# Optimization experiments

Measured on AMD Instinct MI355X. Metric: run time of the kernel, lower is better.

The kernel has to match this reference:

```python
import jax, jax.numpy as jnp
import numpy as np

N_HEAD = 16


def _rope(x, cos, sin):
    # x: [B, T, H, hd]; cos/sin: [1, T, 1, hd//2] (interleaved-pair rotation)
    x1, x2 = x[..., ::2], x[..., 1::2]
    r1 = x1 * cos - x2 * sin
    r2 = x1 * sin + x2 * cos
    return jnp.stack([r1, r2], axis=-1).reshape(x.shape)


def setup_inputs() -> dict:
    key = jax.random.key(0)
    k1, k2, k3 = jax.random.split(key, 3)
    B, T, D = 2, 2048, 2048
    x = jax.random.normal(k1, (B, T, D), dtype=jnp.float32)
    w_attn = jax.random.normal(k2, (3 * D, D), dtype=jnp.float32) * 0.02
    w_proj = jax.random.normal(k3, (D, D), dtype=jnp.float32) * 0.02
    return {"x": x, "w_attn": w_attn, "w_proj": w_proj}


def reference(x, w_attn, w_proj):
    B, T, D = x.shape
    H = N_HEAD
    hd = D // H
    # fused QKV projection (bias=False)
    qkv = x @ w_attn.T                      # [B, T, 3D]
    q, k, v = jnp.split(qkv, 3, axis=-1)
    q = q.reshape(B, T, H, hd)
    k = k.reshape(B, T, H, hd)
    v = v.reshape(B, T, H, hd)
    # RoPE tables: inv_freq = 1/10000^(2i/hd), angles m*theta_i
    inv_freq = 1.0 / (10000.0 ** (jnp.arange(0, hd, 2, dtype=jnp.float32) / hd))
    t = jnp.arange(T, dtype=jnp.float32)
    freqs = t[:, None] * inv_freq[None, :]  # [T, hd//2]
    cos = jnp.cos(freqs)[None, :, None, :]
    sin = jnp.sin(freqs)[None, :, None, :]
    q = _rope(q, cos, sin)
    k = _rope(k, cos, sin)
    # causal attention with materialized [B,H,T,T] scores (as in source)
    scale = 1.0 / np.sqrt(hd).astype(np.float32)
    att = jnp.einsum('bthd,bshd->bhts', q, k) * scale
    causal = jnp.tril(jnp.ones((T, T), dtype=bool))
    att = jnp.where(causal, att, -jnp.inf)
    att = jax.nn.softmax(att, axis=-1)
    y = jnp.einsum('bhts,bshd->bthd', att, v).reshape(B, T, D)
    return y @ w_proj.T
```

## Files before the change

### kernel.cpp

```cpp
#include <hip/hip_runtime.h>
#include <hip/hip_bf16.h>

#define T_SEQ 2048
#define DMODEL 2048
#define NB 2
#define NH 16
#define HD 128

typedef __attribute__((ext_vector_type(8))) short short8;
typedef __attribute__((ext_vector_type(4))) float f32x4;
typedef __attribute__((ext_vector_type(16))) float f32x16;
typedef unsigned short ushort_t;

__device__ inline ushort_t f2bf(float f) {
  union { float f; unsigned u; } v; v.f = f;
  unsigned r = v.u + 0x7fffu + ((v.u >> 16) & 1u);
  return (ushort_t)(r >> 16);
}
__device__ inline float bf2f(ushort_t u) {
  union { unsigned u; float f; } v; v.u = ((unsigned)u) << 16;
  return v.f;
}
__device__ inline unsigned pk2(float x, float y) {
  union { __hip_bfloat162 h; unsigned u; } c;
  c.h = __float22bfloat162_rn(float2{x, y});
  return c.u;
}
__device__ inline float fexp2(float x) {
  float r;
  asm("v_exp_f32 %0, %1" : "=v"(r) : "v"(x));
  return r;
}

__device__ inline void gload16(const void* g, void* l) {
  __builtin_amdgcn_global_load_lds(
      (const __attribute__((address_space(1))) unsigned*)g,
      (__attribute__((address_space(3))) unsigned*)l, 16, 0, 0);
}

__global__ void cvt_f32_bf16(const float* __restrict__ src, ushort_t* __restrict__ dst, int n8) {
  int i = blockIdx.x * blockDim.x + threadIdx.x;
  if (i >= n8) return;
  const float4* s = (const float4*)src + (size_t)i * 2;
  float4 a = s[0], b = s[1];
  short8 o;
  o[0] = (short)f2bf(a.x); o[1] = (short)f2bf(a.y);
  o[2] = (short)f2bf(a.z); o[3] = (short)f2bf(a.w);
  o[4] = (short)f2bf(b.x); o[5] = (short)f2bf(b.y);
  o[6] = (short)f2bf(b.z); o[7] = (short)f2bf(b.w);
  *((short8*)dst + i) = o;
}

__global__ void trig_init(float* __restrict__ trig) {
  int idx = blockIdx.x * blockDim.x + threadIdx.x;
  if (idx >= T_SEQ * 64) return;
  int i = idx & 63, t = idx >> 6;
  float inv = __expf(-(float)i * (9.210340371976184f / 64.0f));
  float f = (float)t * inv;
  trig[idx * 2]     = cosf(f);
  trig[idx * 2 + 1] = sinf(f);
}

__global__ void rope_kernel(ushort_t* __restrict__ q, ushort_t* __restrict__ k,
                            const float* __restrict__ trig) {
  int idx = blockIdx.x * blockDim.x + threadIdx.x;
  int i8 = idx & 15;
  int h  = (idx >> 4) & 15;
  int t  = (idx >> 8) & (T_SEQ - 1);
  int b  = idx >> 19;
  size_t base = ((size_t)((b * NH + h) * T_SEQ + t)) * HD + i8 * 8;
  const float4* tr = (const float4*)(trig + t * 128 + i8 * 8);
  float4 t0 = tr[0], t1 = tr[1];
  float c[4] = { t0.x, t0.z, t1.x, t1.z };
  float s[4] = { t0.y, t0.w, t1.y, t1.w };
  short8 vq = *(short8*)(q + base);
  short8 vk = *(short8*)(k + base);
  short8 oq, ok;
#pragma unroll
  for (int j = 0; j < 4; ++j) {
    float x1 = bf2f((ushort_t)vq[2*j]), x2 = bf2f((ushort_t)vq[2*j+1]);
    oq[2*j]   = (short)f2bf(x1 * c[j] - x2 * s[j]);
    oq[2*j+1] = (short)f2bf(x1 * s[j] + x2 * c[j]);
    x1 = bf2f((ushort_t)vk[2*j]); x2 = bf2f((ushort_t)vk[2*j+1]);
    ok[2*j]   = (short)f2bf(x1 * c[j] - x2 * s[j]);
    ok[2*j+1] = (short)f2bf(x1 * s[j] + x2 * c[j]);
  }
  *(short8*)(q + base) = oq;
  *(short8*)(k + base) = ok;
}

__global__ __launch_bounds__(256)
void v_transpose(const ushort_t* __restrict__ v, ushort_t* __restrict__ vt) {
  __shared__ __align__(16) ushort_t L[64][136];
  int bh = blockIdx.y;
  int t0 = blockIdx.x * 64;
  int tid = threadIdx.x;
  int row = tid >> 2, c0 = (tid & 3) * 32;
  const ushort_t* src = v + ((size_t)bh * T_SEQ + t0 + row) * HD + c0;
#pragma unroll
  for (int j = 0; j < 4; ++j)
    *(short8*)&L[row][c0 + j * 8] = *(const short8*)(src + j * 8);
  __syncthreads();
  int d = tid >> 1, tc = (tid & 1) * 32;
  union { ushort_t u[32]; short8 v8[4]; } buf;
#pragma unroll
  for (int j = 0; j < 32; ++j) buf.u[j] = L[tc + j][d];
  ushort_t* dst = vt + ((size_t)bh * HD + d) * T_SEQ + t0 + tc;
#pragma unroll
  for (int j = 0; j < 4; ++j) *(short8*)(dst + j * 8) = buf.v8[j];
}

template <int EPI>
__global__ __launch_bounds__(256)
void gemm_bt(const ushort_t* __restrict__ A, const ushort_t* __restrict__ Bt,
             float* __restrict__ C, ushort_t* __restrict__ q_t,
             ushort_t* __restrict__ k_t, ushort_t* __restrict__ v_t,
             int M, int N, int K) {
  __shared__ __align__(16) ushort_t As[128 * 32];
  __shared__ __align__(16) ushort_t Bs[128 * 32];
  int tid = threadIdx.x, lane = tid & 63, w = tid >> 6;
  int wm = w >> 1, wn = w & 1;
  int li = lane & 15, lg = lane >> 4;
  int tile_n = blockIdx.x * 128, tile_m = blockIdx.y * 128;
  f32x4 acc[4][4] = {};
  int arow = lane >> 2, acol = (lane & 3) * 8;
  const ushort_t* Ag = A + (size_t)tile_m * K;
  const ushort_t* Bg = Bt + (size_t)tile_n * K;
  for (int k0 = 0; k0 < K; k0 += 32) {
#pragma unroll
    for (int i = 0; i < 2; ++i) {
      int blk = w * 2 + i;
      gload16(Ag + (size_t)(blk * 16 + arow) * K + k0 + acol, &As[blk * 512]);
      gload16(Bg + (size_t)(blk * 16 + arow) * K + k0 + acol, &Bs[blk * 512]);
    }
    __syncthreads();
    short8 af[4], bfr[4];
#pragma unroll
    for (int mi = 0; mi < 4; ++mi)
      af[mi] = *(const short8*)&As[(wm * 64 + mi * 16 + li) * 32 + lg * 8];
#pragma unroll
    for (int ni = 0; ni < 4; ++ni)
      bfr[ni] = *(const short8*)&Bs[(wn * 64 + ni * 16 + li) * 32 + lg * 8];
#pragma unroll
    for (int mi = 0; mi < 4; ++mi)
#pragma unroll
      for (int ni = 0; ni < 4; ++ni)
        acc[mi][ni] = __builtin_amdgcn_mfma_f32_16x16x32_bf16(af[mi], bfr[ni], acc[mi][ni], 0, 0, 0);
    __syncthreads();
  }
#pragma unroll
  for (int mi = 0; mi < 4; ++mi) {
    int row = tile_m + wm * 64 + mi * 16 + lg * 4;
#pragma unroll
    for (int ni = 0; ni < 4; ++ni) {
      int col = tile_n + wn * 64 + ni * 16 + li;
#pragma unroll
      for (int r = 0; r < 4; ++r) {
        float val = acc[mi][ni][r];
        if (EPI == 0) {
          C[(size_t)(row + r) * N + col] = val;
        } else {
          int m = row + r;
          int b = m >> 11, t = m & 2047;
          int sec = col >> 11, nn = col & 2047;
          int h = nn >> 7, d = nn & 127;
          ushort_t* dst = (sec == 0) ? q_t : ((sec == 1) ? k_t : v_t);
          dst[((size_t)((b * NH + h) * T_SEQ + t)) * HD + d] = f2bf(val);
        }
      }
    }
  }
}

__global__ __launch_bounds__(256, 2)
void flash_attn(const ushort_t* __restrict__ Q, const ushort_t* __restrict__ Kg,
                const ushort_t* __restrict__ Vt, ushort_t* __restrict__ Y) {
  __shared__ __align__(16) ushort_t ldsK[2 * 64 * 128];
  __shared__ __align__(16) ushort_t ldsV[2 * 128 * 64];
  int tid = threadIdx.x, lane = tid & 63, w = tid >> 6;
  int hi = lane >> 5, l31 = lane & 31;
  int qi = (blockIdx.y & 16) ? (15 - (int)blockIdx.x) : (int)blockIdx.x;
  int bh = blockIdx.y;
  int b = bh >> 4, h = bh & 15;
  int q0 = qi * 128;
  const ushort_t* Qp = Q + (size_t)bh * T_SEQ * HD;
  const ushort_t* Kp = Kg + (size_t)bh * T_SEQ * HD;
  const ushort_t* Vp = Vt + (size_t)bh * HD * T_SEQ;

  int qg = q0 + w * 32 + l31;
  int qmaxw = q0 + w * 32 + 31;

  auto stage = [&](int kv0, int bsel) {
    ushort_t* Kb = ldsK + bsel * 8192;
    ushort_t* Vb = ldsV + bsel * 8192;
#pragma unroll
    for (int p = 0; p < 4; ++p) {
      int c = p * 256 + w * 64 + lane;
      {
        int row = c >> 4, cc = c & 15;
        int sc = cc ^ (row & 15);
        gload16(Kp + (size_t)(kv0 + row) * HD + sc * 8, Kb + (p * 256 + w * 64) * 8);
      }
      {
        int d = c >> 3, cc = c & 7;
        int sc = cc ^ (d & 7);
        gload16(Vp + (size_t)d * T_SEQ + kv0 + sc * 8, Vb + (p * 256 + w * 64) * 8);
      }
    }
  };

  short8 qf[8];
#pragma unroll
  for (int ds = 0; ds < 8; ++ds)
    qf[ds] = *(const short8*)(Qp + (size_t)qg * HD + ds * 16 + hi * 8);

  f32x16 o[4] = {};
  float mu = -1e30f, l = 0.f;
  const float SIG = 0.12751879523209784f;

  int nkt = 2 * qi + 2;
  stage(0, 0);
  __syncthreads();
  int cur = 0;
  for (int kt = 0; kt < nkt; ++kt) {
    int kv0 = kt * 64;
    if (kt + 1 < nkt) stage((kt + 1) * 64, cur ^ 1);
    if (kv0 <= qmaxw) {
      const ushort_t* Kb = ldsK + cur * 8192;
      const ushort_t* Vb = ldsV + cur * 8192;
      f32x16 sa = {}, sb = {};
      __builtin_amdgcn_s_setprio(1);
#pragma unroll
      for (int ds = 0; ds < 8; ++ds) {
        int cc = ds * 2 + hi;
        short8 k0 = *(const short8*)&Kb[l31 * 128 + ((cc ^ (l31 & 15)) * 8)];
        short8 k1 = *(const short8*)&Kb[(32 + l31) * 128 + ((cc ^ (l31 & 15)) * 8)];
        sa = __builtin_amdgcn_mfma_f32_32x32x16_bf16(k0, qf[ds], sa, 0, 0, 0);
        sb = __builtin_amdgcn_mfma_f32_32x32x16_bf16(k1, qf[ds], sb, 0, 0, 0);
      }
      __builtin_amdgcn_s_setprio(0);
      float p[32];
#pragma unroll
      for (int r = 0; r < 16; ++r) { p[r] = sa[r] * SIG; p[16 + r] = sb[r] * SIG; }
      if (kv0 + 63 > qmaxw - 31 + (l31 - l31)) {
        if (kv0 + 63 > q0 + w * 32) {
#pragma unroll
          for (int r = 0; r < 16; ++r) {
            int loc = (r & 3) + 8 * (r >> 2) + 4 * hi;
            if (kv0 + loc > qg)      p[r]      = -3e38f;
            if (kv0 + 32 + loc > qg) p[16 + r] = -3e38f;
          }
        }
      }
      float tm[16];
#pragma unroll
      for (int i = 0; i < 16; ++i) tm[i] = fmaxf(p[i], p[i + 16]);
#pragma unroll
      for (int st = 8; st >= 1; st >>= 1)
#pragma unroll
        for (int i = 0; i < 8; ++i)
          if (i < st) tm[i] = fmaxf(tm[i], tm[i + st]);
      float pmax = fmaxf(tm[0], __shfl_xor(tm[0], 32));
      bool resc = !__all(pmax <= mu + 11.0f);
      if (resc) {
        float munew = fmaxf(mu, pmax);
        float alpha = fexp2(mu - munew);
        mu = munew;
        l *= alpha;
#pragma unroll
        for (int dsub = 0; dsub < 4; ++dsub)
#pragma unroll
          for (int r = 0; r < 16; ++r) o[dsub][r] *= alpha;
      }
#pragma unroll
      for (int i = 0; i < 32; ++i) p[i] = fexp2(p[i] - mu);
      float ts[16];
#pragma unroll
      for (int i = 0; i < 16; ++i) ts[i] = p[i] + p[i + 16];
#pragma unroll
      for (int st = 8; st >= 1; st >>= 1)
#pragma unroll
        for (int i = 0; i < 8; ++i)
          if (i < st) ts[i] += ts[i + st];
      l += ts[0] + __shfl_xor(ts[0], 32);
      __builtin_amdgcn_s_setprio(1);
#pragma unroll
      for (int s = 0; s < 4; ++s) {
        int rb = (s >> 1) * 16 + (s & 1) * 8;
        unsigned a0 = pk2(p[rb + 0], p[rb + 1]);
        unsigned a1 = pk2(p[rb + 2], p[rb + 3]);
        unsigned a2 = pk2(p[rb + 4], p[rb + 5]);
        unsigned a3 = pk2(p[rb + 6], p[rb + 7]);
        unsigned sa0 = (unsigned)__shfl_xor((int)a0, 32);
        unsigned sa1 = (unsigned)__shfl_xor((int)a1, 32);
        unsigned sa2 = (unsigned)__shfl_xor((int)a2, 32);
        unsigned sa3 = (unsigned)__shfl_xor((int)a3, 32);
        union { unsigned u[4]; short8 s8; } pf;
        pf.u[0] = hi ? sa2 : a0;
        pf.u[1] = hi ? sa3 : a1;
        pf.u[2] = hi ? a2 : sa0;
        pf.u[3] = hi ? a3 : sa1;
#pragma unroll
        for (int dsub = 0; dsub < 4; ++dsub) {
          int row = dsub * 32 + l31;
          short8 vf = *(const short8*)&Vb[row * 64 + (((2 * s + hi) ^ (row & 7)) * 8)];
          o[dsub] = __builtin_amdgcn_mfma_f32_32x32x16_bf16(vf, pf.s8, o[dsub], 0, 0, 0);
        }
      }
      __builtin_amdgcn_s_setprio(0);
    }
    __syncthreads();
    cur ^= 1;
  }
  float invl = 1.f / l;
#pragma unroll
  for (int dsub = 0; dsub < 4; ++dsub)
#pragma unroll
    for (int r = 0; r < 16; ++r) o[dsub][r] *= invl;
#pragma unroll
  for (int dsub = 0; dsub < 4; ++dsub)
#pragma unroll
    for (int r = 0; r < 16; r += 2) {
      int d0 = dsub * 32 + (r & 3) + 8 * (r >> 2) + 4 * hi;
      unsigned u = pk2(o[dsub][r], o[dsub][r + 1]);
      *(unsigned*)&ldsK[w * 4096 + l31 * 128 + (((d0 >> 3) ^ (l31 & 15)) * 8) + (d0 & 7)] = u;
    }
  __syncthreads();
#pragma unroll
  for (int rep = 0; rep < 8; ++rep) {
    int idx = rep * 256 + tid;
    int qg2 = idx >> 4, c = idx & 15;
    int wv2 = qg2 >> 5, ql = qg2 & 31;
    short8 val = *(const short8*)&ldsK[wv2 * 4096 + ql * 128 + ((c ^ (ql & 15)) * 8)];
    *(short8*)(Y + ((size_t)(b * T_SEQ + q0 + qg2)) * DMODEL + h * HD + c * 8) = val;
  }
}

extern "C" void kernel_launch(void* const* d_in, const int* in_sizes, int n_in,
                              void* d_out, int out_size, void* d_ws, size_t ws_size,
                              hipStream_t stream) {
  const float* x      = (const float*)d_in[0];
  const float* w_attn = (const float*)d_in[1];
  const float* w_proj = (const float*)d_in[2];
  float* out = (float*)d_out;

  char* ws = (char*)d_ws;
  size_t off = 0;
  auto alloc = [&](size_t bytes) -> void* {
    void* p = ws + off;
    off = (off + bytes + 255) & ~(size_t)255;
    return p;
  };
  const size_t MT = (size_t)NB * T_SEQ;
  ushort_t* xb   = (ushort_t*)alloc(MT * DMODEL * 2);
  ushort_t* wab  = (ushort_t*)alloc((size_t)3 * DMODEL * DMODEL * 2);
  ushort_t* wpb  = (ushort_t*)alloc((size_t)DMODEL * DMODEL * 2);
  ushort_t* q_t  = (ushort_t*)alloc(MT * DMODEL * 2);
  ushort_t* k_t  = (ushort_t*)alloc(MT * DMODEL * 2);
  ushort_t* v_t  = (ushort_t*)alloc(MT * DMODEL * 2);
  ushort_t* vtb  = (ushort_t*)alloc(MT * DMODEL * 2);
  ushort_t* yb   = (ushort_t*)alloc(MT * DMODEL * 2);
  float*    trig = (float*)alloc((size_t)T_SEQ * 64 * 2 * 4);
  (void)ws_size; (void)n_in; (void)in_sizes; (void)out_size;

  {
    int n8x = (int)(MT * DMODEL / 8);
    hipLaunchKernelGGL(cvt_f32_bf16, dim3((n8x + 255) / 256), dim3(256), 0, stream, x, xb, n8x);
    int n8a = (int)((size_t)3 * DMODEL * DMODEL / 8);
    hipLaunchKernelGGL(cvt_f32_bf16, dim3((n8a + 255) / 256), dim3(256), 0, stream, w_attn, wab, n8a);
    int n8p = (int)((size_t)DMODEL * DMODEL / 8);
    hipLaunchKernelGGL(cvt_f32_bf16, dim3((n8p + 255) / 256), dim3(256), 0, stream, w_proj, wpb, n8p);
  }
  hipLaunchKernelGGL(trig_init, dim3(T_SEQ * 64 / 256), dim3(256), 0, stream, trig);

  hipLaunchKernelGGL((gemm_bt<1>), dim3(3 * DMODEL / 128, MT / 128), dim3(256), 0, stream,
                     xb, wab, (float*)nullptr, q_t, k_t, v_t,
                     (int)MT, 3 * DMODEL, DMODEL);

  hipLaunchKernelGGL(rope_kernel, dim3(NB * T_SEQ * NH * 16 / 256), dim3(256), 0, stream,
                     q_t, k_t, trig);

  hipLaunchKernelGGL(v_transpose, dim3(T_SEQ / 64, NB * NH), dim3(256), 0, stream, v_t, vtb);

  hipLaunchKernelGGL(flash_attn, dim3(T_SEQ / 128, NB * NH), dim3(256), 0, stream,
                     q_t, k_t, vtb, yb);

  hipLaunchKernelGGL((gemm_bt<0>), dim3(DMODEL / 128, MT / 128), dim3(256), 0, stream,
                     yb, wpb, out, (ushort_t*)nullptr, (ushort_t*)nullptr, (ushort_t*)nullptr,
                     (int)MT, DMODEL, DMODEL);
}
```

Before: 322.0 us.

## Fuse RoPE and V transpose into the QKV GEMM epilogue

The QKV projection epilogue now applies RoPE to Q and K in registers, using a lane shuffle to fetch the pair partner and reading cos/sin from the trig table. It also writes V already transposed through a swizzled LDS staging buffer. This removes the separate rope and v_transpose kernels and their extra global read/write passes over Q, K and V. The attention mask condition is also simplified. The cost is a heavier GEMM epilogue with scattered trig loads, and RoPE is now applied to fp32 accumulators before rounding to bf16 instead of to already-rounded bf16 values.

After: 317.8 us. About the same (-1.3%).

```diff
diff --git a/kernel.cpp b/kernel.cpp
--- a/kernel.cpp
+++ b/kernel.cpp
@@ -61,63 +61,15 @@
   trig[idx * 2 + 1] = sinf(f);
 }
 
-__global__ void rope_kernel(ushort_t* __restrict__ q, ushort_t* __restrict__ k,
-                            const float* __restrict__ trig) {
-  int idx = blockIdx.x * blockDim.x + threadIdx.x;
-  int i8 = idx & 15;
-  int h  = (idx >> 4) & 15;
-  int t  = (idx >> 8) & (T_SEQ - 1);
-  int b  = idx >> 19;
-  size_t base = ((size_t)((b * NH + h) * T_SEQ + t)) * HD + i8 * 8;
-  const float4* tr = (const float4*)(trig + t * 128 + i8 * 8);
-  float4 t0 = tr[0], t1 = tr[1];
-  float c[4] = { t0.x, t0.z, t1.x, t1.z };
-  float s[4] = { t0.y, t0.w, t1.y, t1.w };
-  short8 vq = *(short8*)(q + base);
-  short8 vk = *(short8*)(k + base);
-  short8 oq, ok;
-#pragma unroll
-  for (int j = 0; j < 4; ++j) {
-    float x1 = bf2f((ushort_t)vq[2*j]), x2 = bf2f((ushort_t)vq[2*j+1]);
-    oq[2*j]   = (short)f2bf(x1 * c[j] - x2 * s[j]);
-    oq[2*j+1] = (short)f2bf(x1 * s[j] + x2 * c[j]);
-    x1 = bf2f((ushort_t)vk[2*j]); x2 = bf2f((ushort_t)vk[2*j+1]);
-    ok[2*j]   = (short)f2bf(x1 * c[j] - x2 * s[j]);
-    ok[2*j+1] = (short)f2bf(x1 * s[j] + x2 * c[j]);
-  }
-  *(short8*)(q + base) = oq;
-  *(short8*)(k + base) = ok;
-}
-
-__global__ __launch_bounds__(256)
-void v_transpose(const ushort_t* __restrict__ v, ushort_t* __restrict__ vt) {
-  __shared__ __align__(16) ushort_t L[64][136];
-  int bh = blockIdx.y;
-  int t0 = blockIdx.x * 64;
-  int tid = threadIdx.x;
-  int row = tid >> 2, c0 = (tid & 3) * 32;
-  const ushort_t* src = v + ((size_t)bh * T_SEQ + t0 + row) * HD + c0;
-#pragma unroll
-  for (int j = 0; j < 4; ++j)
-    *(short8*)&L[row][c0 + j * 8] = *(const short8*)(src + j * 8);
-  __syncthreads();
-  int d = tid >> 1, tc = (tid & 1) * 32;
-  union { ushort_t u[32]; short8 v8[4]; } buf;
-#pragma unroll
-  for (int j = 0; j < 32; ++j) buf.u[j] = L[tc + j][d];
-  ushort_t* dst = vt + ((size_t)bh * HD + d) * T_SEQ + t0 + tc;
-#pragma unroll
-  for (int j = 0; j < 4; ++j) *(short8*)(dst + j * 8) = buf.v8[j];
-}
-
 template <int EPI>
 __global__ __launch_bounds__(256)
 void gemm_bt(const ushort_t* __restrict__ A, const ushort_t* __restrict__ Bt,
              float* __restrict__ C, ushort_t* __restrict__ q_t,
-             ushort_t* __restrict__ k_t, ushort_t* __restrict__ v_t,
-             int M, int N, int K) {
-  __shared__ __align__(16) ushort_t As[128 * 32];
-  __shared__ __align__(16) ushort_t Bs[128 * 32];
+             ushort_t* __restrict__ k_t, ushort_t* __restrict__ vt,
+             const float* __restrict__ trig, int M, int N, int K) {
+  __shared__ __align__(16) ushort_t smem[8192];
+  ushort_t* As = smem;
+  ushort_t* Bs = smem + 4096;
   int tid = threadIdx.x, lane = tid & 63, w = tid >> 6;
   int wm = w >> 1, wn = w & 1;
   int li = lane & 15, lg = lane >> 4;
@@ -148,24 +100,72 @@
         acc[mi][ni] = __builtin_amdgcn_mfma_f32_16x16x32_bf16(af[mi], bfr[ni], acc[mi][ni], 0, 0, 0);
     __syncthreads();
   }
-#pragma unroll
-  for (int mi = 0; mi < 4; ++mi) {
-    int row = tile_m + wm * 64 + mi * 16 + lg * 4;
-#pragma unroll
-    for (int ni = 0; ni < 4; ++ni) {
-      int col = tile_n + wn * 64 + ni * 16 + li;
-#pragma unroll
-      for (int r = 0; r < 4; ++r) {
-        float val = acc[mi][ni][r];
-        if (EPI == 0) {
-          C[(size_t)(row + r) * N + col] = val;
-        } else {
-          int m = row + r;
-          int b = m >> 11, t = m & 2047;
-          int sec = col >> 11, nn = col & 2047;
-          int h = nn >> 7, d = nn & 127;
-          ushort_t* dst = (sec == 0) ? q_t : ((sec == 1) ? k_t : v_t);
-          dst[((size_t)((b * NH + h) * T_SEQ + t)) * HD + d] = f2bf(val);
+
+  if (EPI == 0) {
+#pragma unroll
+    for (int mi = 0; mi < 4; ++mi) {
+      int row = tile_m + wm * 64 + mi * 16 + lg * 4;
+#pragma unroll
+      for (int ni = 0; ni < 4; ++ni) {
+        int col = tile_n + wn * 64 + ni * 16 + li;
+#pragma unroll
+        for (int r = 0; r < 4; ++r)
+          C[(size_t)(row + r) * N + col] = acc[mi][ni][r];
+      }
+    }
+  } else {
+    int sec = tile_n >> 11;
+    int nn  = tile_n & 2047;
+    int h   = nn >> 7;
+    int bq  = tile_m >> 11;
+    int t0  = tile_m & 2047;
+    if (sec < 2) {
+      ushort_t* dst = (sec == 0) ? q_t : k_t;
+      ushort_t* base = dst + ((size_t)(bq * NH + h)) * T_SEQ * HD;
+#pragma unroll
+      for (int mi = 0; mi < 4; ++mi) {
+        int tl = wm * 64 + mi * 16 + lg * 4;
+#pragma unroll
+        for (int ni = 0; ni < 4; ++ni) {
+          int d = wn * 64 + ni * 16 + li;
+          int fi = d >> 1;
+#pragma unroll
+          for (int r = 0; r < 4; ++r) {
+            int t = t0 + tl + r;
+            float val = acc[mi][ni][r];
+            float par = __shfl_xor(val, 1);
+            const float* tp = trig + t * 128 + fi * 2;
+            float c = tp[0], s = tp[1];
+            float out = (li & 1) ? (par * s + val * c) : (val * c - par * s);
+            base[(size_t)t * HD + d] = f2bf(out);
+          }
+        }
+      }
+    } else {
+      ushort_t* vbase = vt + ((size_t)(bq * NH + h)) * HD * T_SEQ;
+#pragma unroll
+      for (int c = 0; c < 2; ++c) {
+        __syncthreads();
+        if (wm == c) {
+#pragma unroll
+          for (int mi = 0; mi < 4; ++mi)
+#pragma unroll
+            for (int ni = 0; ni < 4; ++ni) {
+              int d = wn * 64 + ni * 16 + li;
+#pragma unroll
+              for (int r = 0; r < 4; ++r) {
+                int tl = mi * 16 + lg * 4 + r;
+                smem[d * 64 + (tl ^ ((d & 7) << 3))] = f2bf(acc[mi][ni][r]);
+              }
+            }
+        }
+        __syncthreads();
+#pragma unroll
+        for (int j = 0; j < 4; ++j) {
+          int idx = j * 256 + tid;
+          int d = idx >> 3, tg = idx & 7;
+          short8 val = *(const short8*)&smem[d * 64 + ((tg * 8) ^ ((d & 7) << 3))];
+          *(short8*)(vbase + (size_t)d * T_SEQ + t0 + c * 64 + tg * 8) = val;
         }
       }
     }
@@ -242,14 +242,12 @@
       float p[32];
 #pragma unroll
       for (int r = 0; r < 16; ++r) { p[r] = sa[r] * SIG; p[16 + r] = sb[r] * SIG; }
-      if (kv0 + 63 > qmaxw - 31 + (l31 - l31)) {
-        if (kv0 + 63 > q0 + w * 32) {
-#pragma unroll
-          for (int r = 0; r < 16; ++r) {
-            int loc = (r & 3) + 8 * (r >> 2) + 4 * hi;
-            if (kv0 + loc > qg)      p[r]      = -3e38f;
-            if (kv0 + 32 + loc > qg) p[16 + r] = -3e38f;
-          }
+      if (kv0 + 63 > q0 + w * 32) {
+#pragma unroll
+        for (int r = 0; r < 16; ++r) {
+          int loc = (r & 3) + 8 * (r >> 2) + 4 * hi;
+          if (kv0 + loc > qg)      p[r]      = -3e38f;
+          if (kv0 + 32 + loc > qg) p[16 + r] = -3e38f;
         }
       }
       float tm[16];
@@ -357,7 +355,6 @@
   ushort_t* wpb  = (ushort_t*)alloc((size_t)DMODEL * DMODEL * 2);
   ushort_t* q_t  = (ushort_t*)alloc(MT * DMODEL * 2);
   ushort_t* k_t  = (ushort_t*)alloc(MT * DMODEL * 2);
-  ushort_t* v_t  = (ushort_t*)alloc(MT * DMODEL * 2);
   ushort_t* vtb  = (ushort_t*)alloc(MT * DMODEL * 2);
   ushort_t* yb   = (ushort_t*)alloc(MT * DMODEL * 2);
   float*    trig = (float*)alloc((size_t)T_SEQ * 64 * 2 * 4);
@@ -374,18 +371,13 @@
   hipLaunchKernelGGL(trig_init, dim3(T_SEQ * 64 / 256), dim3(256), 0, stream, trig);
 
   hipLaunchKernelGGL((gemm_bt<1>), dim3(3 * DMODEL / 128, MT / 128), dim3(256), 0, stream,
-                     xb, wab, (float*)nullptr, q_t, k_t, v_t,
+                     xb, wab, (float*)nullptr, q_t, k_t, vtb, trig,
                      (int)MT, 3 * DMODEL, DMODEL);
-
-  hipLaunchKernelGGL(rope_kernel, dim3(NB * T_SEQ * NH * 16 / 256), dim3(256), 0, stream,
-                     q_t, k_t, trig);
-
-  hipLaunchKernelGGL(v_transpose, dim3(T_SEQ / 64, NB * NH), dim3(256), 0, stream, v_t, vtb);
 
   hipLaunchKernelGGL(flash_attn, dim3(T_SEQ / 128, NB * NH), dim3(256), 0, stream,
                      q_t, k_t, vtb, yb);
 
   hipLaunchKernelGGL((gemm_bt<0>), dim3(DMODEL / 128, MT / 128), dim3(256), 0, stream,
                      yb, wpb, out, (ushort_t*)nullptr, (ushort_t*)nullptr, (ushort_t*)nullptr,
-                     (int)MT, DMODEL, DMODEL);
-}
+                     (const float*)nullptr, (int)MT, DMODEL, DMODEL);
+}
```
